# Kernel optimization log

Measured on AMD Instinct MI355X. Metric: run time of the kernel, lower is better.

Reference implementation:

```python
import jax, jax.numpy as jnp
import numpy as np

# dims
B, S, T, F = 8, 1024, 32, 64       # batch, stocks(nodes), seq_len, feature
DWV = 64                            # d_word_vec == d_model
RNN = 64                            # GRU hidden (rnn_unit)
NHID = 128                          # n_hid
NH, DK, DV = 4, 16, 16              # heads, d_k, d_v
NC, NE = 2, 128                     # n_class, num hyperedges (H.shape[1])


def setup_inputs() -> dict:
    key = jax.random.key(0)
    ks = jax.random.split(key, 24)
    def p(i, shape):
        return jax.random.normal(ks[i], shape, jnp.float32) / np.float32(np.sqrt(shape[-1]))
    return {
        'src_seq': jax.random.normal(ks[0], (B, S, T, F), jnp.float32),
        'H': jax.random.normal(ks[1], (S, NE), jnp.float32) * 0.1,
        'adj': jax.random.normal(ks[2], (S, S), jnp.float32) * 0.02,
        'n_hid': NHID,
        # GCN (feature -> n_hid -> feature), shared across both adj and H_new branches
        'gcn_W1': p(3, (F, NHID)), 'gcn_b1': jnp.zeros((NHID,), jnp.float32),
        'gcn_W2': p(4, (NHID, F)), 'gcn_b2': jnp.zeros((F,), jnp.float32),
        # Linear(H.shape[1] -> H.shape[0]) created inside forward
        'Wm': p(5, (S, NE)) * 0.1, 'bm': jnp.zeros((S,), jnp.float32),
        # Linear(feature -> d_word_vec)
        'Wl': p(6, (DWV, F)), 'bl': jnp.zeros((DWV,), jnp.float32),
        # 2-layer GRU (batch_first), torch layout W_{ir|iz|in} stacked
        'Wx0': p(7, (3 * RNN, DWV)), 'Wh0': p(8, (3 * RNN, RNN)),
        'bx0': jnp.zeros((3 * RNN,), jnp.float32), 'bh0': jnp.zeros((3 * RNN,), jnp.float32),
        'Wx1': p(9, (3 * RNN, RNN)), 'Wh1': p(10, (3 * RNN, RNN)),
        'bx1': jnp.zeros((3 * RNN,), jnp.float32), 'bh1': jnp.zeros((3 * RNN,), jnp.float32),
        # temporal multi-head attention
        'Wq': p(11, (NH * DK, RNN)), 'Wk': p(12, (NH * DK, RNN)), 'Wv': p(13, (NH * DV, RNN)),
        'Wo': p(14, (RNN, NH * DV)),
        'ln_g': jnp.ones((RNN,), jnp.float32), 'ln_b': jnp.zeros((RNN,), jnp.float32),
        # HGN: two graph-conv layers over stocks, (T*RNN -> n_hid -> n_hid)
        'Wg1': p(15, (T * RNN, NHID)), 'Wg2': p(16, (NHID, NHID)),
        # tgt_word_prj: n_hid -> n_class (no bias)
        'Wp': p(17, (NC, NHID)),
    }


def reference(src_seq, H, adj, n_hid, gcn_W1, gcn_b1, gcn_W2, gcn_b2, Wm, bm,
              Wl, bl, Wx0, Wh0, bx0, bh0, Wx1, Wh1, bx1, bh1,
              Wq, Wk, Wv, Wo, ln_g, ln_b, Wg1, Wg2, Wp):
    b, s, t, f = src_seq.shape

    # per-timestep GCN over the stock (node) axis, fully batched (replaces the
    # double Python loop of mm+spmm in the original)
    def gcn(x, A):  # x: (b,s,t,f), A: (s,s)
        h = jax.nn.relu(jnp.einsum('nm,bmth->bnth', A, x @ gcn_W1) + gcn_b1)
        return jnp.einsum('nm,bmtf->bntf', A, h @ gcn_W2) + gcn_b2

    H_new = H @ Wm.T + bm                       # (s,s) learned hypergraph adjacency
    z = gcn(src_seq, adj) + gcn(src_seq, H_new)  # y_i + y_f for all timesteps

    x = (z @ Wl.T + bl).reshape(b * s, t, -1)    # (N, T, DWV)
    n = b * s

    def gru_layer(xin, Wx, Wh, bx, bh):
        hdim = Wh.shape[1]
        xp = xin @ Wx.T + bx                      # precompute input projections (N,T,3H)
        def step(h, xt):
            gh = h @ Wh.T + bh
            xr, xz, xn = jnp.split(xt, 3, -1)
            hr, hz, hn = jnp.split(gh, 3, -1)
            r = jax.nn.sigmoid(xr + hr)
            zg = jax.nn.sigmoid(xz + hz)
            cand = jnp.tanh(xn + r * hn)
            hnew = (1.0 - zg) * cand + zg * h
            return hnew, hnew
        h0 = jnp.zeros((xin.shape[0], hdim), xin.dtype)
        _, ys = jax.lax.scan(step, h0, jnp.swapaxes(xp, 0, 1))
        return jnp.swapaxes(ys, 0, 1)

    r = gru_layer(gru_layer(x, Wx0, Wh0, bx0, bh0), Wx1, Wh1, bx1, bh1)  # (N,T,RNN)

    # temporal multi-head self-attention with causal (subsequent) mask
    q = (r @ Wq.T).reshape(n, t, NH, DK)
    k = (r @ Wk.T).reshape(n, t, NH, DK)
    v = (r @ Wv.T).reshape(n, t, NH, DV)
    scores = jnp.einsum('nqhd,nkhd->nhqk', q, k) / np.float32(np.sqrt(DK))
    causal = jnp.triu(jnp.ones((t, t), bool), 1)
    attn = jax.nn.softmax(jnp.where(causal, jnp.float32(-1e9), scores), -1)
    o = jnp.einsum('nhqk,nkhd->nqhd', attn, v).reshape(n, t, NH * DV) @ Wo.T + r
    mu = o.mean(-1, keepdims=True)
    o = (o - mu) / jnp.sqrt(o.var(-1, keepdims=True) + 1e-6) * ln_g + ln_b

    enc = o.reshape(b, s, t * o.shape[-1])        # (b, s, T*RNN)

    # HGN: two graph convolutions over the stock axis -> (b, s, n_hid)
    hg = jax.nn.relu(jnp.einsum('nm,bmd->bnd', adj, enc @ Wg1))
    hg = jnp.einsum('nm,bmd->bnd', adj, hg @ Wg2)

    return hg.reshape(b * s, -1) @ Wp.T           # x_logit_scale = 1.0 (no weight sharing)
```

## Files before the change

kernel.cpp:

```cpp
#include <hip/hip_runtime.h>

typedef __attribute__((ext_vector_type(8))) short bf8;
typedef __attribute__((ext_vector_type(4))) float f4;

__device__ __forceinline__ ushort f2b(float f) {
  union { float f; unsigned u; } v; v.f = f;
  unsigned u = v.u + 0x7FFFu + ((v.u >> 16) & 1u);
  return (ushort)(u >> 16);
}
__device__ __forceinline__ float b2f(ushort h) {
  union { unsigned u; float f; } v; v.u = ((unsigned)h) << 16; return v.f;
}
__device__ __forceinline__ bf8 pack8(const float* p) {
  f4 a = *(const f4*)p; f4 b = *(const f4*)(p + 4);
  bf8 t;
  t[0] = (short)f2b(a[0]); t[1] = (short)f2b(a[1]);
  t[2] = (short)f2b(a[2]); t[3] = (short)f2b(a[3]);
  t[4] = (short)f2b(b[0]); t[5] = (short)f2b(b[1]);
  t[6] = (short)f2b(b[2]); t[7] = (short)f2b(b[3]);
  return t;
}
__device__ __forceinline__ float sigm(float x) { return 1.f / (1.f + __expf(-x)); }
__device__ __forceinline__ float tanh_f(float x) {
  float a = fabsf(x), e = __expf(-2.f * a);
  return copysignf((1.f - e) / (1.f + e), x);
}

__device__ __forceinline__ void gl16(const void* g, void* l) {
  __builtin_amdgcn_global_load_lds(
      (const __attribute__((address_space(1))) unsigned int*)(uintptr_t)g,
      (__attribute__((address_space(3))) unsigned int*)(uintptr_t)l, 16, 0, 0);
}

#define SFENCE __builtin_amdgcn_sched_barrier(0)
#define RAWBAR { __builtin_amdgcn_s_barrier(); SFENCE; }
#define WAIT_LGKM0 { asm volatile("s_waitcnt lgkmcnt(0)" ::: "memory"); SFENCE; }
#define WAIT_VM(n) { asm volatile("s_waitcnt vmcnt(" #n ")" ::: "memory"); SFENCE; }

__global__ __launch_bounds__(256) void cvt_k(const float* __restrict__ in,
                                             ushort* __restrict__ out, int n4) {
  int i = blockIdx.x * 256 + threadIdx.x;
  if (i < n4) {
    f4 v = ((const f4*)in)[i];
    ushort4 o;
    o.x = f2b(v[0]); o.y = f2b(v[1]); o.z = f2b(v[2]); o.w = f2b(v[3]);
    ((ushort4*)out)[i] = o;
  }
}

__global__ __launch_bounds__(256) void cvtT_k(const float* __restrict__ in,
                                              ushort* __restrict__ out, int R, int C) {
  __shared__ ushort t[64][68];
  const int tid = threadIdx.x;
  const int r0 = blockIdx.x * 64, c0 = blockIdx.y * 64;
  #pragma unroll
  for (int it = 0; it < 4; ++it) {
    int r = (tid >> 4) + 16 * it, c = (tid & 15) * 4;
    f4 v = *(const f4*)(in + (long)(r0 + r) * C + c0 + c);
    #pragma unroll
    for (int j = 0; j < 4; ++j) t[c + j][r] = f2b(v[j]);
  }
  __syncthreads();
  #pragma unroll
  for (int it = 0; it < 4; ++it) {
    int cc = (tid >> 4) + 16 * it, rr = (tid & 15) * 4;
    ushort4 o = { t[cc][rr], t[cc][rr + 1], t[cc][rr + 2], t[cc][rr + 3] };
    *(ushort4*)(out + (long)(c0 + cc) * R + r0 + rr) = o;
  }
}

__global__ __launch_bounds__(256) void cat_k(const ushort* __restrict__ a,
                                             const ushort* __restrict__ h,
                                             ushort* __restrict__ o) {
  int i = blockIdx.x * 256 + threadIdx.x;
  int s = i >> 7, c8 = (i & 127) << 3;
  *(int4*)(o + (long)s * 2048 + c8) = *(const int4*)(a + (long)s * 1024 + c8);
  *(int4*)(o + (long)s * 2048 + 1024 + c8) = *(const int4*)(h + (long)s * 1024 + c8);
}

__global__ void wcombT_k(const float* __restrict__ Wl, const float* __restrict__ W2,
                         ushort* __restrict__ out) {
  int idx = blockIdx.x * 256 + threadIdx.x;
  int d = idx >> 7, h = idx & 127;
  float s = 0.f;
  #pragma unroll
  for (int f = 0; f < 64; ++f) s += Wl[d * 64 + f] * W2[h * 64 + f];
  out[d * 128 + h] = f2b(s);
}
__global__ void biasc_k(const float* __restrict__ gb2, const float* __restrict__ Wl,
                        const float* __restrict__ bl, float* __restrict__ bc) {
  int d = threadIdx.x;
  float s = 0.f;
  #pragma unroll
  for (int f = 0; f < 64; ++f) s += gb2[f] * Wl[d * 64 + f];
  bc[d] = 2.f * s + bl[d];
}
__global__ void wfin_k(const float* __restrict__ Wg2, const float* __restrict__ Wp,
                       float* __restrict__ wf) {
  int idx = threadIdx.x;
  int d = idx >> 1, c = idx & 1;
  float s = 0.f;
  #pragma unroll
  for (int e = 0; e < 128; ++e) s += Wg2[d * 128 + e] * Wp[c * 128 + e];
  wf[idx] = s;
}

template<int BIASMODE, int RELU, int OUTMODE>
__global__ __launch_bounds__(512, 2) void gemm3_k(
    const ushort* __restrict__ A, const ushort* __restrict__ B,
    ushort* __restrict__ C, const float* __restrict__ bias, int biasMask,
    int N, int K, int lda, int ldb, int ldc,
    long sAq, long sBq, long sCq)
{
  __shared__ __align__(16) ushort As[2 * 256 * 64];
  __shared__ __align__(16) ushort Bs[2 * 256 * 64];
  const int tid = threadIdx.x, lane = tid & 63, wv = tid >> 6;
  const int wm = wv >> 2, wn = wv & 3;
  const long bm = (long)blockIdx.x * 256, bn = (long)blockIdx.y * 256;
  const int z = blockIdx.z;
  const ushort* Ap = A + (long)z * sAq + bm * lda;
  const ushort* Bp = B + (long)z * sBq + bn * ldb;
  ushort* Cp = C + (long)z * sCq;
  const int nt = K >> 6;

  const int srow = wv * 32 + (lane >> 3);
  const int scol = ((lane & 7) ^ (srow & 7)) << 3;
  const ushort* apb = Ap + (long)srow * lda + scol;
  const ushort* bpb = Bp + (long)srow * ldb + scol;

  #define STAGE3(T, D) { \
    const ushort* ap_ = apb + (T) * 64; \
    const ushort* bp_ = bpb + (T) * 64; \
    ushort* la_ = &As[(D) * 16384 + (wv * 32) * 64]; \
    ushort* lb_ = &Bs[(D) * 16384 + (wv * 32) * 64]; \
    _Pragma("unroll") \
    for (int i_ = 0; i_ < 4; ++i_) gl16(ap_ + (long)(i_ * 8) * lda, la_ + i_ * 512); \
    _Pragma("unroll") \
    for (int i_ = 0; i_ < 4; ++i_) gl16(bp_ + (long)(i_ * 8) * ldb, lb_ + i_ * 512); \
  }

  STAGE3(0, 0);
  if (nt > 1) { STAGE3(1, 1); WAIT_VM(8); }
  else        { WAIT_VM(0); }
  RAWBAR;

  f4 acc[8][4] = {};
  for (int t = 0; t < nt; ++t) {
    const int d = t & 1;
    const ushort* as = As + d * 16384;
    const ushort* bs = Bs + d * 16384;
    bf8 b0[4], a0[8];
    #pragma unroll
    for (int n = 0; n < 4; ++n) {
      int r = wn * 64 + n * 16 + (lane & 15);
      b0[n] = *(const bf8*)(bs + r * 64 + (((lane >> 4) ^ (r & 7)) << 3));
    }
    #pragma unroll
    for (int m = 0; m < 8; ++m) {
      int r = wm * 128 + m * 16 + (lane & 15);
      a0[m] = *(const bf8*)(as + r * 64 + (((lane >> 4) ^ (r & 7)) << 3));
    }
    __builtin_amdgcn_s_setprio(1);
    #pragma unroll
    for (int m = 0; m < 8; ++m)
      #pragma unroll
      for (int n = 0; n < 4; ++n)
        acc[m][n] = __builtin_amdgcn_mfma_f32_16x16x32_bf16(a0[m], b0[n], acc[m][n], 0, 0, 0);
    __builtin_amdgcn_s_setprio(0);
    bf8 b1[4], a1[8];
    #pragma unroll
    for (int n = 0; n < 4; ++n) {
      int r = wn * 64 + n * 16 + (lane & 15);
      b1[n] = *(const bf8*)(bs + r * 64 + (((4 + (lane >> 4)) ^ (r & 7)) << 3));
    }
    #pragma unroll
    for (int m = 0; m < 8; ++m) {
      int r = wm * 128 + m * 16 + (lane & 15);
      a1[m] = *(const bf8*)(as + r * 64 + (((4 + (lane >> 4)) ^ (r & 7)) << 3));
    }
    WAIT_LGKM0;
    RAWBAR;
    if (t + 2 < nt) STAGE3(t + 2, d);
    __builtin_amdgcn_s_setprio(1);
    #pragma unroll
    for (int m = 0; m < 8; ++m)
      #pragma unroll
      for (int n = 0; n < 4; ++n)
        acc[m][n] = __builtin_amdgcn_mfma_f32_16x16x32_bf16(a1[m], b1[n], acc[m][n], 0, 0, 0);
    __builtin_amdgcn_s_setprio(0);
    if (t + 1 < nt) {
      if (t + 2 < nt) { WAIT_VM(8); }
      else            { WAIT_VM(0); }
      RAWBAR;
    }
  }
  #undef STAGE3

  #pragma unroll
  for (int m = 0; m < 8; ++m) {
    int grow = (int)bm + wm * 128 + m * 16 + ((lane >> 4) << 2);
    #pragma unroll
    for (int n = 0; n < 4; ++n) {
      int col = (int)bn + wn * 64 + n * 16 + (lane & 15);
      if (OUTMODE == 2) {
        int hh = grow & 127, tt = grow >> 7;
        ushort4 o;
        o.x = f2b(acc[m][n][0]); o.y = f2b(acc[m][n][1]);
        o.z = f2b(acc[m][n][2]); o.w = f2b(acc[m][n][3]);
        *(ushort4*)(Cp + ((long)col * 32 + tt) * 128 + hh) = o;
      } else {
        #pragma unroll
        for (int rr = 0; rr < 4; ++rr) {
          float v = acc[m][n][rr];
          if (BIASMODE == 1) v += bias[col & biasMask];
          if (BIASMODE == 2) v += bias[(grow + rr) & biasMask];
          if (RELU) v = fmaxf(v, 0.f);
          Cp[(long)(grow + rr) * ldc + col] = f2b(v);
        }
      }
    }
  }
}

template<int BIASMODE, int RELU, int OUTMODE, int SWZ>
__global__ __launch_bounds__(256) void gemm2_k(
    const ushort* __restrict__ A, const ushort* __restrict__ B,
    ushort* __restrict__ C, const float* __restrict__ bias, int biasMask,
    int N, int K, int lda, int ldb, int ldc, int ZD,
    long sAq, long sAr, long sBq, long sBr, long sCq, long sCr)
{
  __shared__ __align__(16) ushort As[2 * 128 * 64];
  __shared__ __align__(16) ushort Bs[2 * 128 * 64];
  const int tid = threadIdx.x, lane = tid & 63, wv = tid >> 6;
  const int wm = wv >> 1, wn = wv & 1;
  int bx = blockIdx.x, by = blockIdx.y;
  const long bm = (long)bx * 128, bn = (long)by * 128;
  int z = blockIdx.z, zq = z, zr = 0;
  if (ZD > 1) { zq = z / ZD; zr = z - zq * ZD; }
  const ushort* Ap = A + (long)zq * sAq + (long)zr * sAr + bm * lda;
  const ushort* Bp = B + (long)zq * sBq + (long)zr * sBr + bn * ldb;
  ushort* Cp = C + (long)zq * sCq + (long)zr * sCr;
  const int nt = K >> 6;

  const int srow = wv * 32 + (lane >> 3);
  const int scol = ((lane & 7) ^ (srow & 7)) << 3;
  const ushort* apb = Ap + (long)srow * lda + scol;
  const ushort* bpb = Bp + (long)srow * ldb + scol;

  #define STAGE(T, D) { \
    const ushort* ap_ = apb + (T) * 64; \
    const ushort* bp_ = bpb + (T) * 64; \
    ushort* la_ = &As[((D) * 128 + wv * 32) * 64]; \
    ushort* lb_ = &Bs[((D) * 128 + wv * 32) * 64]; \
    _Pragma("unroll") \
    for (int i_ = 0; i_ < 4; ++i_) gl16(ap_ + (long)(i_ * 8) * lda, la_ + i_ * 512); \
    _Pragma("unroll") \
    for (int i_ = 0; i_ < 4; ++i_) gl16(bp_ + (long)(i_ * 8) * ldb, lb_ + i_ * 512); \
  }

  STAGE(0, 0);
  if (nt > 1) { STAGE(1, 1); WAIT_VM(8); }
  else        { WAIT_VM(0); }
  RAWBAR;

  f4 acc[4][4] = {};
  for (int t = 0; t < nt; ++t) {
    const int d = t & 1;
    const ushort* as = As + d * 8192;
    const ushort* bs = Bs + d * 8192;
    bf8 af[4][2], bfv[4][2];
    #pragma unroll
    for (int mi = 0; mi < 4; ++mi) {
      int r = wm * 64 + mi * 16 + (lane & 15);
      #pragma unroll
      for (int kk = 0; kk < 2; ++kk) {
        int blk = kk * 4 + (lane >> 4);
        af[mi][kk] = *(const bf8*)(as + r * 64 + ((blk ^ (r & 7)) << 3));
      }
    }
    #pragma unroll
    for (int ni = 0; ni < 4; ++ni) {
      int r = wn * 64 + ni * 16 + (lane & 15);
      #pragma unroll
      for (int kk = 0; kk < 2; ++kk) {
        int blk = kk * 4 + (lane >> 4);
        bfv[ni][kk] = *(const bf8*)(bs + r * 64 + ((blk ^ (r & 7)) << 3));
      }
    }
    WAIT_LGKM0;
    RAWBAR;
    if (t + 2 < nt) STAGE(t + 2, d);
    #pragma unroll
    for (int kk = 0; kk < 2; ++kk)
      #pragma unroll
      for (int mi = 0; mi < 4; ++mi)
        #pragma unroll
        for (int ni = 0; ni < 4; ++ni)
          acc[mi][ni] = __builtin_amdgcn_mfma_f32_16x16x32_bf16(af[mi][kk], bfv[ni][kk], acc[mi][ni], 0, 0, 0);
    if (t + 1 < nt) {
      if (t + 2 < nt) { WAIT_VM(8); }
      else            { WAIT_VM(0); }
      RAWBAR;
    }
  }
  #undef STAGE

  #pragma unroll
  for (int mi = 0; mi < 4; ++mi)
    #pragma unroll
    for (int ni = 0; ni < 4; ++ni) {
      int col = (int)bn + wn * 64 + ni * 16 + (lane & 15);
      if (col < N) {
        if (OUTMODE == 2) {
          int hh = wm * 64 + mi * 16 + (lane >> 4) * 4;
          int tt = (int)(bm >> 7);
          ushort4 o;
          o.x = f2b(acc[mi][ni][0]); o.y = f2b(acc[mi][ni][1]);
          o.z = f2b(acc[mi][ni][2]); o.w = f2b(acc[mi][ni][3]);
          *(ushort4*)(Cp + ((long)col * 32 + tt) * 128 + hh) = o;
        } else {
          #pragma unroll
          for (int rr = 0; rr < 4; ++rr) {
            int row = (int)bm + wm * 64 + mi * 16 + (lane >> 4) * 4 + rr;
            float v = acc[mi][ni][rr];
            if (BIASMODE == 1) v += bias[col & biasMask];
            if (BIASMODE == 2) v += bias[row & biasMask];
            if (RELU) v = fmaxf(v, 0.f);
            Cp[(long)row * ldc + col] = f2b(v);
          }
        }
      }
    }
}

__global__ __launch_bounds__(256) void gemmsk_k(
    const ushort* __restrict__ A, const ushort* __restrict__ B,
    float* __restrict__ P, int Kc, int lda, int ldb,
    long sAq, long sBq)
{
  __shared__ __align__(16) ushort As[2 * 128 * 64];
  __shared__ __align__(16) ushort Bs[2 * 128 * 64];
  const int tid = threadIdx.x, lane = tid & 63, wv = tid >> 6;
  const int wm = wv >> 1, wn = wv & 1;
  const long bm = (long)blockIdx.x * 128, bn = (long)blockIdx.y * 128;
  const int kc = blockIdx.z & 3, zq = blockIdx.z >> 2;
  const ushort* Ap = A + (long)zq * sAq + kc * Kc + bm * lda;
  const ushort* Bp = B + (long)zq * sBq + kc * Kc + bn * ldb;
  const int nt = Kc >> 6;

  const int srow = wv * 32 + (lane >> 3);
  const int scol = ((lane & 7) ^ (srow & 7)) << 3;
  const ushort* apb = Ap + (long)srow * lda + scol;
  const ushort* bpb = Bp + (long)srow * ldb + scol;

  #define STAGEK(T, D) { \
    const ushort* ap_ = apb + (T) * 64; \
    const ushort* bp_ = bpb + (T) * 64; \
    ushort* la_ = &As[((D) * 128 + wv * 32) * 64]; \
    ushort* lb_ = &Bs[((D) * 128 + wv * 32) * 64]; \
    _Pragma("unroll") \
    for (int i_ = 0; i_ < 4; ++i_) gl16(ap_ + (long)(i_ * 8) * lda, la_ + i_ * 512); \
    _Pragma("unroll") \
    for (int i_ = 0; i_ < 4; ++i_) gl16(bp_ + (long)(i_ * 8) * ldb, lb_ + i_ * 512); \
  }

  STAGEK(0, 0);
  if (nt > 1) { STAGEK(1, 1); WAIT_VM(8); }
  else        { WAIT_VM(0); }
  RAWBAR;

  f4 acc[4][4] = {};
  for (int t = 0; t < nt; ++t) {
    const int d = t & 1;
    const ushort* as = As + d * 8192;
    const ushort* bs = Bs + d * 8192;
    bf8 af[4][2], bfv[4][2];
    #pragma unroll
    for (int mi = 0; mi < 4; ++mi) {
      int r = wm * 64 + mi * 16 + (lane & 15);
      #pragma unroll
      for (int kk = 0; kk < 2; ++kk) {
        int blk = kk * 4 + (lane >> 4);
        af[mi][kk] = *(const bf8*)(as + r * 64 + ((blk ^ (r & 7)) << 3));
      }
    }
    #pragma unroll
    for (int ni = 0; ni < 4; ++ni) {
      int r = wn * 64 + ni * 16 + (lane & 15);
      #pragma unroll
      for (int kk = 0; kk < 2; ++kk) {
        int blk = kk * 4 + (lane >> 4);
        bfv[ni][kk] = *(const bf8*)(bs + r * 64 + ((blk ^ (r & 7)) << 3));
      }
    }
    WAIT_LGKM0;
    RAWBAR;
    if (t + 2 < nt) STAGEK(t + 2, d);
    #pragma unroll
    for (int kk = 0; kk < 2; ++kk)
      #pragma unroll
      for (int mi = 0; mi < 4; ++mi)
        #pragma unroll
        for (int ni = 0; ni < 4; ++ni)
          acc[mi][ni] = __builtin_amdgcn_mfma_f32_16x16x32_bf16(af[mi][kk], bfv[ni][kk], acc[mi][ni], 0, 0, 0);
    if (t + 1 < nt) {
      if (t + 2 < nt) { WAIT_VM(8); }
      else            { WAIT_VM(0); }
      RAWBAR;
    }
  }
  #undef STAGEK

  float* Pp = P + (long)blockIdx.z * 131072;
  #pragma unroll
  for (int mi = 0; mi < 4; ++mi)
    #pragma unroll
    for (int ni = 0; ni < 4; ++ni) {
      int col = (int)bn + wn * 64 + ni * 16 + (lane & 15);
      #pragma unroll
      for (int rr = 0; rr < 4; ++rr) {
        int row = (int)bm + wm * 64 + mi * 16 + (lane >> 4) * 4 + rr;
        Pp[(long)row * 1024 + col] = acc[mi][ni][rr];
      }
    }
}

template<int RELU>
__global__ __launch_bounds__(256) void redk_k(const float* __restrict__ P,
                                              ushort* __restrict__ C) {
  int idx = blockIdx.x * 256 + threadIdx.x;
  long z = idx >> 15;
  long rem = (long)(idx & 32767) * 4;
  const float* base = P + z * 4 * 131072 + rem;
  f4 s = *(const f4*)base;
  #pragma unroll
  for (int kc = 1; kc < 4; ++kc) s += *(const f4*)(base + kc * 131072);
  ushort4 o;
  #pragma unroll
  for (int j = 0; j < 4; ++j) {
    float v = s[j];
    if (RELU) v = fmaxf(v, 0.f);
    ((ushort*)&o)[j] = f2b(v);
  }
  *(ushort4*)(C + z * 131072 + rem) = o;
}

template<int BIASMODE, int RELU, int FULLB, int OUTMODE, int SWZ>
__global__ __launch_bounds__(256) void gemm_k(
    const ushort* __restrict__ A, const ushort* __restrict__ B,
    ushort* __restrict__ C, const float* __restrict__ bias, int biasMask,
    int N, int K, int lda, int ldb, int ldc, int ZD,
    long sAq, long sAr, long sBq, long sBr, long sCq, long sCr)
{
  __shared__ __align__(16) ushort As[128 * 64];
  __shared__ __align__(16) ushort Bs[128 * 64];
  const int tid = threadIdx.x, lane = tid & 63, wv = tid >> 6;
  const int wm = wv >> 1, wn = wv & 1;
  int bx = blockIdx.x, by = blockIdx.y;
  const long bm = (long)bx * 128, bn = (long)by * 128;
  int z = blockIdx.z, zq = z, zr = 0;
  if (ZD > 1) { zq = z / ZD; zr = z - zq * ZD; }
  const ushort* Ap = A + (long)zq * sAq + (long)zr * sAr + bm * lda;
  const ushort* Bp = B + (long)zq * sBq + (long)zr * sBr + bn * ldb;
  ushort* Cp = C + (long)zq * sCq + (long)zr * sCr;
  f4 acc[4][4] = {};
  for (int k0 = 0; k0 < K; k0 += 64) {
    #pragma unroll
    for (int i = 0; i < 4; ++i) {
      int row = wv * 32 + i * 8 + (lane >> 3);
      int gc = k0 + (((lane & 7) ^ (row & 7)) << 3);
      gl16(Ap + (long)row * lda + gc, &As[(wv * 32 + i * 8) * 64]);
    }
    if (FULLB) {
      #pragma unroll
      for (int i = 0; i < 4; ++i) {
        int row = wv * 32 + i * 8 + (lane >> 3);
        int gc = k0 + (((lane & 7) ^ (row & 7)) << 3);
        gl16(Bp + (long)row * ldb + gc, &Bs[(wv * 32 + i * 8) * 64]);
      }
    } else {
      #pragma unroll
      for (int i = 0; i < 4; ++i) {
        int row = (tid >> 3) + 32 * i;
        int b8 = tid & 7;
        int4 v = {0, 0, 0, 0};
        if (bn + row < N) v = *(const int4*)(Bp + (long)row * ldb + k0 + ((b8 ^ (row & 7)) << 3));
        *(int4*)(&Bs[row * 64 + b8 * 8]) = v;
      }
    }
    __syncthreads();
    bf8 af[4][2], bfv[4][2];
    #pragma unroll
    for (int mi = 0; mi < 4; ++mi) {
      int r = wm * 64 + mi * 16 + (lane & 15);
      #pragma unroll
      for (int kk = 0; kk < 2; ++kk) {
        int blk = kk * 4 + (lane >> 4);
        af[mi][kk] = *(const bf8*)(&As[r * 64 + ((blk ^ (r & 7)) << 3)]);
      }
    }
    #pragma unroll
    for (int ni = 0; ni < 4; ++ni) {
      int r = wn * 64 + ni * 16 + (lane & 15);
      #pragma unroll
      for (int kk = 0; kk < 2; ++kk) {
        int blk = kk * 4 + (lane >> 4);
        bfv[ni][kk] = *(const bf8*)(&Bs[r * 64 + ((blk ^ (r & 7)) << 3)]);
      }
    }
    #pragma unroll
    for (int kk = 0; kk < 2; ++kk)
      #pragma unroll
      for (int mi = 0; mi < 4; ++mi)
        #pragma unroll
        for (int ni = 0; ni < 4; ++ni)
          acc[mi][ni] = __builtin_amdgcn_mfma_f32_16x16x32_bf16(af[mi][kk], bfv[ni][kk], acc[mi][ni], 0, 0, 0);
    __syncthreads();
  }
  #pragma unroll
  for (int mi = 0; mi < 4; ++mi)
    #pragma unroll
    for (int ni = 0; ni < 4; ++ni) {
      int col = (int)bn + wn * 64 + ni * 16 + (lane & 15);
      if (col < N) {
        #pragma unroll
        for (int rr = 0; rr < 4; ++rr) {
          int row = (int)bm + wm * 64 + mi * 16 + (lane >> 4) * 4 + rr;
          float v = acc[mi][ni][rr];
          if (BIASMODE == 1) v += bias[col & biasMask];
          if (BIASMODE == 2) v += bias[row & biasMask];
          if (RELU) v = fmaxf(v, 0.f);
          long oidx;
          if (OUTMODE == 1) oidx = ((long)(row & 31) * 8192 + (row >> 5)) * 64 + col;
          else              oidx = (long)row * ldc + col;
          Cp[oidx] = f2b(v);
        }
      }
    }
}

__global__ __launch_bounds__(256, 2) void gru_k(
    const ushort* __restrict__ xT,
    const float* __restrict__ Wx0, const float* __restrict__ Wh0,
    const float* __restrict__ bx0, const float* __restrict__ bh0,
    const float* __restrict__ Wx1, const float* __restrict__ Wh1,
    const float* __restrict__ bx1, const float* __restrict__ bh1,
    ushort* __restrict__ rout)
{
  __shared__ ushort hbf[2][2][1024];
  const int tid = threadIdx.x, lane = tid & 63, w = tid >> 6;
  const int seq0 = blockIdx.x * 16;
  for (int i = tid; i < 4096; i += 256) ((ushort*)hbf)[i] = 0;

  const float* Wxp[2] = {Wx0, Wx1};
  const float* Whp[2] = {Wh0, Wh1};
  const float* bxp[2] = {bx0, bx1};
  const float* bhp[2] = {bh0, bh1};
  bf8 Wxf[2][3][2], Whf[2][3][2];
  float bxv[2][3], bhv[2][3];
  #pragma unroll
  for (int L = 0; L < 2; ++L)
    #pragma unroll
    for (int g = 0; g < 3; ++g) {
      int row = g * 64 + w * 16 + (lane & 15);
      bxv[L][g] = bxp[L][row];
      bhv[L][g] = bhp[L][row];
      #pragma unroll
      for (int kk = 0; kk < 2; ++kk) {
        int kb = kk * 32 + (lane >> 4) * 8;
        Wxf[L][g][kk] = pack8(Wxp[L] + row * 64 + kb);
        Whf[L][g][kk] = pack8(Whp[L] + row * 64 + kb);
      }
    }
  __syncthreads();

  const int arow = lane & 15;
  const int col = w * 16 + (lane & 15);
  f4 hprev[2] = {{0.f,0.f,0.f,0.f},{0.f,0.f,0.f,0.f}};
  int pv = 0;
  for (int t = 0; t < 32; ++t) {
    const int cur = pv ^ 1;
    #pragma unroll
    for (int L = 0; L < 2; ++L) {
      bf8 axf[2], ahf[2];
      if (L == 0) {
        const ushort* xb = xT + ((long)t * 8192 + seq0 + arow) * 64 + (lane >> 4) * 8;
        axf[0] = *(const bf8*)(xb);
        axf[1] = *(const bf8*)(xb + 32);
      } else {
        #pragma unroll
        for (int kk = 0; kk < 2; ++kk) {
          int blk = kk * 4 + (lane >> 4);
          axf[kk] = *(const bf8*)(&hbf[0][cur][arow * 64 + ((blk ^ (arow & 7)) << 3)]);
        }
      }
      #pragma unroll
      for (int kk = 0; kk < 2; ++kk) {
        int blk = kk * 4 + (lane >> 4);
        ahf[kk] = *(const bf8*)(&hbf[L][pv][arow * 64 + ((blk ^ (arow & 7)) << 3)]);
      }
      f4 aX[3] = {}; f4 aH[3] = {};
      #pragma unroll
      for (int kk = 0; kk < 2; ++kk)
        #pragma unroll
        for (int g = 0; g < 3; ++g) {
          aX[g] = __builtin_amdgcn_mfma_f32_16x16x32_bf16(axf[kk], Wxf[L][g][kk], aX[g], 0, 0, 0);
          aH[g] = __builtin_amdgcn_mfma_f32_16x16x32_bf16(ahf[kk], Whf[L][g][kk], aH[g], 0, 0, 0);
        }
      f4 hn;
      #pragma unroll
      for (int r = 0; r < 4; ++r) {
        float rg = sigm(aX[0][r] + bxv[L][0] + aH[0][r] + bhv[L][0]);
        float zg = sigm(aX[1][r] + bxv[L][1] + aH[1][r] + bhv[L][1]);
        float cand = tanh_f(aX[2][r] + bxv[L][2] + rg * (aH[2][r] + bhv[L][2]));
        hn[r] = (1.f - zg) * cand + zg * hprev[L][r];
      }
      hprev[L] = hn;
      #pragma unroll
      for (int r = 0; r < 4; ++r) {
        int row = (lane >> 4) * 4 + r;
        ushort hb = f2b(hn[r]);
        hbf[L][cur][row * 64 + (((col >> 3) ^ (row & 7)) << 3) + (col & 7)] = hb;
        if (L == 1) rout[((long)(seq0 + row) * 32 + t) * 64 + col] = hb;
      }
      __syncthreads();
    }
    pv = cur;
  }
}

__global__ __launch_bounds__(256) void attn_k(
    const ushort* __restrict__ r,
    const float* __restrict__ Wq, const float* __restrict__ Wk,
    const float* __restrict__ Wv, const float* __restrict__ Wo,
    const float* __restrict__ lng, const float* __restrict__ lnb,
    ushort* __restrict__ enc)
{
  __shared__ ushort q_s[4][32][40];
  __shared__ ushort k_s[4][32][40];
  __shared__ ushort v_s[4][16][40];
  __shared__ ushort p_s[4][32][40];
  __shared__ ushort o_s[32][88];
  __shared__ float  ln_s[32][68];
  const int tid = threadIdx.x, lane = tid & 63, w = tid >> 6;
  const long n = blockIdx.x;

  for (int i = tid; i < 4 * 32 * 40; i += 256) { ((ushort*)q_s)[i] = 0; ((ushort*)k_s)[i] = 0; }

  bf8 wqf[2], wkf[2], wvf[2], wof[2];
  #pragma unroll
  for (int kk = 0; kk < 2; ++kk) {
    int row = w * 16 + (lane & 15);
    int kb = kk * 32 + (lane >> 4) * 8;
    wqf[kk] = pack8(Wq + row * 64 + kb);
    wkf[kk] = pack8(Wk + row * 64 + kb);
    wvf[kk] = pack8(Wv + row * 64 + kb);
    wof[kk] = pack8(Wo + row * 64 + kb);
  }
  __syncthreads();

  bf8 ar[2][2];
  #pragma unroll
  for (int mi = 0; mi < 2; ++mi)
    #pragma unroll
    for (int kk = 0; kk < 2; ++kk)
      ar[mi][kk] = *(const bf8*)(r + (n * 32 + mi * 16 + (lane & 15)) * 64 + kk * 32 + (lane >> 4) * 8);
  f4 aq[2] = {}, ak[2] = {}, av[2] = {};
  #pragma unroll
  for (int kk = 0; kk < 2; ++kk)
    #pragma unroll
    for (int mi = 0; mi < 2; ++mi) {
      aq[mi] = __builtin_amdgcn_mfma_f32_16x16x32_bf16(ar[mi][kk], wqf[kk], aq[mi], 0, 0, 0);
      ak[mi] = __builtin_amdgcn_mfma_f32_16x16x32_bf16(ar[mi][kk], wkf[kk], ak[mi], 0, 0, 0);
      av[mi] = __builtin_amdgcn_mfma_f32_16x16x32_bf16(ar[mi][kk], wvf[kk], av[mi], 0, 0, 0);
    }
  #pragma unroll
  for (int mi = 0; mi < 2; ++mi)
    #pragma unroll
    for (int rr = 0; rr < 4; ++rr) {
      int row = mi * 16 + (lane >> 4) * 4 + rr;
      q_s[w][row][lane & 15] = f2b(aq[mi][rr]);
      k_s[w][row][lane & 15] = f2b(ak[mi][rr]);
      v_s[w][lane & 15][row] = f2b(av[mi][rr]);
    }

  bf8 a_q[2], b_k[2];
  #pragma unroll
  for (int mt = 0; mt < 2; ++mt)
    a_q[mt] = *(const bf8*)(&q_s[w][mt * 16 + (lane & 15)][(lane >> 4) * 8]);
  #pragma unroll
  for (int nt = 0; nt < 2; ++nt)
    b_k[nt] = *(const bf8*)(&k_s[w][nt * 16 + (lane & 15)][(lane >> 4) * 8]);
  f4 s_[2][2] = {};
  #pragma unroll
  for (int mt = 0; mt < 2; ++mt)
    #pragma unroll
    for (int nt = 0; nt < 2; ++nt)
      s_[mt][nt] = __builtin_amdgcn_mfma_f32_16x16x32_bf16(a_q[mt], b_k[nt], s_[mt][nt], 0, 0, 0);
  #pragma unroll
  for (int mt = 0; mt < 2; ++mt)
    #pragma unroll
    for (int rr = 0; rr < 4; ++rr) {
      int trow = mt * 16 + (lane >> 4) * 4 + rr;
      float s0 = s_[mt][0][rr] * 0.25f, s1 = s_[mt][1][rr] * 0.25f;
      int c0 = lane & 15, c1 = 16 + (lane & 15);
      if (c0 > trow) s0 = -1e30f;
      if (c1 > trow) s1 = -1e30f;
      float m = fmaxf(s0, s1);
      #pragma unroll
      for (int d = 1; d < 16; d <<= 1) m = fmaxf(m, __shfl_xor(m, d));
      float e0 = __expf(s0 - m), e1 = __expf(s1 - m);
      float sum = e0 + e1;
      #pragma unroll
      for (int d = 1; d < 16; d <<= 1) sum += __shfl_xor(sum, d);
      float inv = 1.f / sum;
      p_s[w][trow][c0] = f2b(e0 * inv);
      p_s[w][trow][c1] = f2b(e1 * inv);
    }

  bf8 b_v = *(const bf8*)(&v_s[w][lane & 15][(lane >> 4) * 8]);
  f4 o_[2] = {};
  #pragma unroll
  for (int mt = 0; mt < 2; ++mt) {
    bf8 a_p = *(const bf8*)(&p_s[w][mt * 16 + (lane & 15)][(lane >> 4) * 8]);
    o_[mt] = __builtin_amdgcn_mfma_f32_16x16x32_bf16(a_p, b_v, o_[mt], 0, 0, 0);
  }
  #pragma unroll
  for (int mt = 0; mt < 2; ++mt)
    #pragma unroll
    for (int rr = 0; rr < 4; ++rr)
      o_s[mt * 16 + (lane >> 4) * 4 + rr][w * 16 + (lane & 15)] = f2b(o_[mt][rr]);
  __syncthreads();

  bf8 a_o[2][2];
  #pragma unroll
  for (int mt = 0; mt < 2; ++mt)
    #pragma unroll
    for (int kk = 0; kk < 2; ++kk)
      a_o[mt][kk] = *(const bf8*)(&o_s[mt * 16 + (lane & 15)][kk * 32 + (lane >> 4) * 8]);
  f4 oo[2] = {};
  #pragma unroll
  for (int kk = 0; kk < 2; ++kk)
    #pragma unroll
    for (int mt = 0; mt < 2; ++mt)
      oo[mt] = __builtin_amdgcn_mfma_f32_16x16x32_bf16(a_o[mt][kk], wof[kk], oo[mt], 0, 0, 0);
  #pragma unroll
  for (int mt = 0; mt < 2; ++mt)
    #pragma unroll
    for (int rr = 0; rr < 4; ++rr) {
      int row = mt * 16 + (lane >> 4) * 4 + rr;
      int col = w * 16 + (lane & 15);
      float resid = b2f(r[(n * 32 + row) * 64 + col]);
      ln_s[row][col] = oo[mt][rr] + resid;
    }
  __syncthreads();

  {
    int row = tid >> 3, seg = tid & 7;
    float vals[8], sm = 0.f, sq = 0.f;
    #pragma unroll
    for (int j = 0; j < 8; ++j) {
      float v = ln_s[row][seg * 8 + j];
      vals[j] = v; sm += v; sq += v * v;
    }
    #pragma unroll
    for (int d = 1; d < 8; d <<= 1) { sm += __shfl_xor(sm, d); sq += __shfl_xor(sq, d); }
    float mu = sm * (1.f / 64.f);
    float var = sq * (1.f / 64.f) - mu * mu;
    float rs = rsqrtf(var + 1e-6f);
    union { ushort u[8]; int4 v; } ou;
    #pragma unroll
    for (int j = 0; j < 8; ++j) {
      int c = seg * 8 + j;
      ou.u[j] = f2b((vals[j] - mu) * rs * lng[c] + lnb[c]);
    }
    *(int4*)(enc + (n * 32 + row) * 64 + seg * 8) = ou.v;
  }
}

__global__ __launch_bounds__(256) void final2_k(const ushort* __restrict__ hg3aT,
                                                const float* __restrict__ wf,
                                                float* __restrict__ out) {
  int i = blockIdx.x * 256 + threadIdx.x;
  int b = i >> 10, s = i & 1023;
  const ushort* base = hg3aT + (long)b * 131072 + s;
  float a0 = 0.f, a1 = 0.f;
  #pragma unroll
  for (int d = 0; d < 128; ++d) {
    float v = b2f(base[d * 1024]);
    a0 += v * wf[2 * d];
    a1 += v * wf[2 * d + 1];
  }
  out[2 * i] = a0; out[2 * i + 1] = a1;
}

extern "C" void kernel_launch(void* const* d_in, const int* in_sizes, int n_in,
                              void* d_out, int out_size, void* d_ws, size_t ws_size,
                              hipStream_t stream) {
  const float* src = (const float*)d_in[0];
  const float* H   = (const float*)d_in[1];
  const float* adj = (const float*)d_in[2];
  const float* gW1 = (const float*)d_in[4];
  const float* gb1 = (const float*)d_in[5];
  const float* gW2 = (const float*)d_in[6];
  const float* gb2 = (const float*)d_in[7];
  const float* Wm  = (const float*)d_in[8];
  const float* bm  = (const float*)d_in[9];
  const float* Wl  = (const float*)d_in[10];
  const float* bl  = (const float*)d_in[11];
  const float* Wx0 = (const float*)d_in[12];
  const float* Wh0 = (const float*)d_in[13];
  const float* bx0 = (const float*)d_in[14];
  const float* bh0 = (const float*)d_in[15];
  const float* Wx1 = (const float*)d_in[16];
  const float* Wh1 = (const float*)d_in[17];
  const float* bx1 = (const float*)d_in[18];
  const float* bh1 = (const float*)d_in[19];
  const float* Wq  = (const float*)d_in[20];
  const float* Wk  = (const float*)d_in[21];
  const float* Wv  = (const float*)d_in[22];
  const float* Wo  = (const float*)d_in[23];
  const float* lng = (const float*)d_in[24];
  const float* lnb = (const float*)d_in[25];
  const float* Wg1 = (const float*)d_in[26];
  const float* Wg2 = (const float*)d_in[27];
  const float* Wp  = (const float*)d_in[28];

  char* ws = (char*)d_ws;
  const size_t MB = 1048576ull;
  ushort* adj_bf  = (ushort*)(ws);
  ushort* Hnew_bf = (ushort*)(ws + 2 * MB);
  ushort* H_bf    = (ushort*)(ws + 4 * MB);
  ushort* Wm_bf   = (ushort*)(ws + 4 * MB + 262144);
  ushort* W1T     = (ushort*)(ws + 4 * MB + 524288);
  ushort* WcT     = (ushort*)(ws + 4 * MB + 524288 + 16384);
  float*  bc      = (float*) (ws + 4 * MB + 524288 + 32768);
  float*  wfin    = (float*) (ws + 4 * MB + 524288 + 33792);
  ushort* Wg1T    = (ushort*)(ws + 5 * MB);
  ushort* src_bf  = (ushort*)(ws + 6 * MB);
  ushort* adjcat  = (ushort*)(ws + 6 * MB);
  ushort* XT      = (ushort*)(ws + 38 * MB);
  ushort* Psum    = (ushort*)(ws + 38 * MB);
  float*  Pk      = (float*) (ws + 38 * MB);
  ushort* h1cat   = (ushort*)(ws + 102 * MB);
  ushort* enc     = (ushort*)(ws + 102 * MB);
  ushort* g1T     = (ushort*)(ws + 134 * MB);
  ushort* hgT     = (ushort*)(ws + 136 * MB);
  ushort* hg3aT   = (ushort*)(ws + 138 * MB);
  ushort* xT      = (ushort*)(ws + 166 * MB);
  ushort* r_bf    = (ushort*)(ws + 198 * MB);

  auto CVT = [&](const float* in, ushort* out, int n) {
    int n4 = n >> 2;
    cvt_k<<<dim3((n4 + 255) / 256), dim3(256), 0, stream>>>(in, out, n4);
  };
  CVT(src, src_bf, 16777216);
  CVT(adj, adj_bf, 1048576);
  CVT(H, H_bf, 131072);
  CVT(Wm, Wm_bf, 131072);
  cvtT_k<<<dim3(1, 2), 256, 0, stream>>>(gW1, W1T, 64, 128);
  cvtT_k<<<dim3(32, 2), 256, 0, stream>>>(Wg1, Wg1T, 2048, 128);
  wcombT_k<<<dim3(32), 256, 0, stream>>>(Wl, gW2, WcT);
  biasc_k<<<dim3(1), 64, 0, stream>>>(gb2, Wl, bl, bc);
  wfin_k<<<dim3(1), 256, 0, stream>>>(Wg2, Wp, wfin);

  gemm2_k<1,0,0,0><<<dim3(8,8,1),256,0,stream>>>(H_bf, Wm_bf, Hnew_bf, bm, 1023,
      1024, 128, 128, 128, 1024, 1, 0,0, 0,0, 0,0);
  gemm2_k<0,0,0,0><<<dim3(1,8,256),256,0,stream>>>(W1T, src_bf, XT, nullptr, 0,
      1024, 64, 64, 2048, 1024, 32, 0,0, 2097152,64, 4194304,131072);
  cat_k<<<dim3(512),256,0,stream>>>(adj_bf, Hnew_bf, adjcat);
  gemm3_k<2,1,0><<<dim3(16,8,8),512,0,stream>>>(XT, adj_bf, h1cat, gb1, 127,
      2048, 1024, 1024, 1024, 2048, 4194304, 0, 8388608);
  gemm3_k<0,0,2><<<dim3(16,4,8),512,0,stream>>>(h1cat, adjcat, Psum, nullptr, 0,
      1024, 2048, 2048, 2048, 0, 8388608, 0, 4194304);
  gemm_k<1,0,0,1,0><<<dim3(2048,1,1),256,0,stream>>>(Psum, WcT, xT, bc, 63,
      64, 128, 128, 128, 64, 1, 0,0, 0,0, 0,0);
  gru_k<<<dim3(512),dim3(256),0,stream>>>(xT, Wx0,Wh0,bx0,bh0, Wx1,Wh1,bx1,bh1, r_bf);
  attn_k<<<dim3(8192),dim3(256),0,stream>>>(r_bf, Wq,Wk,Wv,Wo, lng,lnb, enc);
  gemmsk_k<<<dim3(1,8,32),256,0,stream>>>(Wg1T, enc, Pk, 512, 2048, 2048, 0, 2097152);
  redk_k<0><<<dim3(1024),256,0,stream>>>(Pk, g1T);
  gemmsk_k<<<dim3(1,8,32),256,0,stream>>>(g1T, adj_bf, Pk, 256, 1024, 1024, 131072, 0);
  redk_k<1><<<dim3(1024),256,0,stream>>>(Pk, hgT);
  gemmsk_k<<<dim3(1,8,32),256,0,stream>>>(hgT, adj_bf, Pk, 256, 1024, 1024, 131072, 0);
  redk_k<0><<<dim3(1024),256,0,stream>>>(Pk, hg3aT);
  final2_k<<<dim3(32),256,0,stream>>>(hg3aT, wfin, (float*)d_out);
}
```

Measured before the change: 610.8 us.

## Fuse Wc projection into gemm3 epilogue, dropping Psum intermediate and gemm_k

The second gemm3 launch now has an OUTMODE 3 epilogue. It writes its accumulator tile to LDS, multiplies it by the combined WcT weights with MFMA, adds the bias and stores straight into the GRU input layout xT. This removes the bf16 Psum round trip through global memory and one kernel launch. The cost is extra LDS traffic, a barrier and more register pressure in the big GEMM's epilogue. The workspace buffers are also reshuffled.

```diff
diff --git a/kernel.cpp b/kernel.cpp
--- a/kernel.cpp
+++ b/kernel.cpp
@@ -110,7 +110,8 @@
     const ushort* __restrict__ A, const ushort* __restrict__ B,
     ushort* __restrict__ C, const float* __restrict__ bias, int biasMask,
     int N, int K, int lda, int ldb, int ldc,
-    long sAq, long sBq, long sCq)
+    long sAq, long sBq, long sCq,
+    const ushort* __restrict__ Wc, const float* __restrict__ bcp)
 {
   __shared__ __align__(16) ushort As[2 * 256 * 64];
   __shared__ __align__(16) ushort Bs[2 * 256 * 64];
@@ -196,19 +197,67 @@
   }
   #undef STAGE3
 
-  #pragma unroll
-  for (int m = 0; m < 8; ++m) {
-    int grow = (int)bm + wm * 128 + m * 16 + ((lane >> 4) << 2);
-    #pragma unroll
-    for (int n = 0; n < 4; ++n) {
-      int col = (int)bn + wn * 64 + n * 16 + (lane & 15);
-      if (OUTMODE == 2) {
-        int hh = grow & 127, tt = grow >> 7;
-        ushort4 o;
-        o.x = f2b(acc[m][n][0]); o.y = f2b(acc[m][n][1]);
-        o.z = f2b(acc[m][n][2]); o.w = f2b(acc[m][n][3]);
-        *(ushort4*)(Cp + ((long)col * 32 + tt) * 128 + hh) = o;
-      } else {
+  if (OUTMODE == 3) {
+    ushort* Ps = (wm == 0) ? (ushort*)As : (ushort*)Bs;
+    #pragma unroll
+    for (int m = 0; m < 8; ++m) {
+      int hq = m * 16 + ((lane >> 4) << 2);
+      #pragma unroll
+      for (int n = 0; n < 4; ++n) {
+        int s = wn * 64 + n * 16 + (lane & 15);
+        int key = (s & 7) << 4;
+        #pragma unroll
+        for (int rr = 0; rr < 4; ++rr)
+          Ps[s * 128 + ((hq + rr) ^ key)] = f2b(acc[m][n][rr]);
+      }
+    }
+    WAIT_LGKM0;
+    RAWBAR;
+    const int tl = wm, sq = wn;
+    const ushort* Pw = (tl == 0) ? (const ushort*)As : (const ushort*)Bs;
+    const int sbase = sq * 64;
+    f4 xacc[4][4] = {};
+    #pragma unroll
+    for (int kk = 0; kk < 4; ++kk) {
+      bf8 pa[4], wb[4];
+      int hq = kk * 32 + ((lane >> 4) << 3);
+      #pragma unroll
+      for (int mt = 0; mt < 4; ++mt) {
+        int s = sbase + mt * 16 + (lane & 15);
+        pa[mt] = *(const bf8*)(Pw + s * 128 + (hq ^ ((s & 7) << 4)));
+      }
+      #pragma unroll
+      for (int ntt = 0; ntt < 4; ++ntt) {
+        int dd = ntt * 16 + (lane & 15);
+        wb[ntt] = *(const bf8*)(Wc + dd * 128 + hq);
+      }
+      #pragma unroll
+      for (int mt = 0; mt < 4; ++mt)
+        #pragma unroll
+        for (int ntt = 0; ntt < 4; ++ntt)
+          xacc[mt][ntt] = __builtin_amdgcn_mfma_f32_16x16x32_bf16(pa[mt], wb[ntt], xacc[mt][ntt], 0, 0, 0);
+    }
+    const int tg = (int)(bm >> 7) + tl;
+    #pragma unroll
+    for (int mt = 0; mt < 4; ++mt)
+      #pragma unroll
+      for (int ntt = 0; ntt < 4; ++ntt) {
+        int dd = ntt * 16 + (lane & 15);
+        float bb = bcp[dd];
+        #pragma unroll
+        for (int rr = 0; rr < 4; ++rr) {
+          int s = sbase + mt * 16 + ((lane >> 4) << 2) + rr;
+          long seq = (long)z * 1024 + bn + s;
+          C[((long)tg * 8192 + seq) * 64 + dd] = f2b(xacc[mt][ntt][rr] + bb);
+        }
+      }
+  } else {
+    #pragma unroll
+    for (int m = 0; m < 8; ++m) {
+      int grow = (int)bm + wm * 128 + m * 16 + ((lane >> 4) << 2);
+      #pragma unroll
+      for (int n = 0; n < 4; ++n) {
+        int col = (int)bn + wn * 64 + n * 16 + (lane & 15);
         #pragma unroll
         for (int rr = 0; rr < 4; ++rr) {
           float v = acc[m][n][rr];
@@ -443,100 +492,6 @@
     ((ushort*)&o)[j] = f2b(v);
   }
   *(ushort4*)(C + z * 131072 + rem) = o;
-}
-
-template<int BIASMODE, int RELU, int FULLB, int OUTMODE, int SWZ>
-__global__ __launch_bounds__(256) void gemm_k(
-    const ushort* __restrict__ A, const ushort* __restrict__ B,
-    ushort* __restrict__ C, const float* __restrict__ bias, int biasMask,
-    int N, int K, int lda, int ldb, int ldc, int ZD,
-    long sAq, long sAr, long sBq, long sBr, long sCq, long sCr)
-{
-  __shared__ __align__(16) ushort As[128 * 64];
-  __shared__ __align__(16) ushort Bs[128 * 64];
-  const int tid = threadIdx.x, lane = tid & 63, wv = tid >> 6;
-  const int wm = wv >> 1, wn = wv & 1;
-  int bx = blockIdx.x, by = blockIdx.y;
-  const long bm = (long)bx * 128, bn = (long)by * 128;
-  int z = blockIdx.z, zq = z, zr = 0;
-  if (ZD > 1) { zq = z / ZD; zr = z - zq * ZD; }
-  const ushort* Ap = A + (long)zq * sAq + (long)zr * sAr + bm * lda;
-  const ushort* Bp = B + (long)zq * sBq + (long)zr * sBr + bn * ldb;
-  ushort* Cp = C + (long)zq * sCq + (long)zr * sCr;
-  f4 acc[4][4] = {};
-  for (int k0 = 0; k0 < K; k0 += 64) {
-    #pragma unroll
-    for (int i = 0; i < 4; ++i) {
-      int row = wv * 32 + i * 8 + (lane >> 3);
-      int gc = k0 + (((lane & 7) ^ (row & 7)) << 3);
-      gl16(Ap + (long)row * lda + gc, &As[(wv * 32 + i * 8) * 64]);
-    }
-    if (FULLB) {
-      #pragma unroll
-      for (int i = 0; i < 4; ++i) {
-        int row = wv * 32 + i * 8 + (lane >> 3);
-        int gc = k0 + (((lane & 7) ^ (row & 7)) << 3);
-        gl16(Bp + (long)row * ldb + gc, &Bs[(wv * 32 + i * 8) * 64]);
-      }
-    } else {
-      #pragma unroll
-      for (int i = 0; i < 4; ++i) {
-        int row = (tid >> 3) + 32 * i;
-        int b8 = tid & 7;
-        int4 v = {0, 0, 0, 0};
-        if (bn + row < N) v = *(const int4*)(Bp + (long)row * ldb + k0 + ((b8 ^ (row & 7)) << 3));
-        *(int4*)(&Bs[row * 64 + b8 * 8]) = v;
-      }
-    }
-    __syncthreads();
-    bf8 af[4][2], bfv[4][2];
-    #pragma unroll
-    for (int mi = 0; mi < 4; ++mi) {
-      int r = wm * 64 + mi * 16 + (lane & 15);
-      #pragma unroll
-      for (int kk = 0; kk < 2; ++kk) {
-        int blk = kk * 4 + (lane >> 4);
-        af[mi][kk] = *(const bf8*)(&As[r * 64 + ((blk ^ (r & 7)) << 3)]);
-      }
-    }
-    #pragma unroll
-    for (int ni = 0; ni < 4; ++ni) {
-      int r = wn * 64 + ni * 16 + (lane & 15);
-      #pragma unroll
-      for (int kk = 0; kk < 2; ++kk) {
-        int blk = kk * 4 + (lane >> 4);
-        bfv[ni][kk] = *(const bf8*)(&Bs[r * 64 + ((blk ^ (r & 7)) << 3)]);
-      }
-    }
-    #pragma unroll
-    for (int kk = 0; kk < 2; ++kk)
-      #pragma unroll
-      for (int mi = 0; mi < 4; ++mi)
-        #pragma unroll
-        for (int ni = 0; ni < 4; ++ni)
-          acc[mi][ni] = __builtin_amdgcn_mfma_f32_16x16x32_bf16(af[mi][kk], bfv[ni][kk], acc[mi][ni], 0, 0, 0);
-    __syncthreads();
-  }
-  #pragma unroll
-  for (int mi = 0; mi < 4; ++mi)
-    #pragma unroll
-    for (int ni = 0; ni < 4; ++ni) {
-      int col = (int)bn + wn * 64 + ni * 16 + (lane & 15);
-      if (col < N) {
-        #pragma unroll
-        for (int rr = 0; rr < 4; ++rr) {
-          int row = (int)bm + wm * 64 + mi * 16 + (lane >> 4) * 4 + rr;
-          float v = acc[mi][ni][rr];
-          if (BIASMODE == 1) v += bias[col & biasMask];
-          if (BIASMODE == 2) v += bias[row & biasMask];
-          if (RELU) v = fmaxf(v, 0.f);
-          long oidx;
-          if (OUTMODE == 1) oidx = ((long)(row & 31) * 8192 + (row >> 5)) * 64 + col;
-          else              oidx = (long)row * ldc + col;
-          Cp[oidx] = f2b(v);
-        }
-      }
-    }
 }
 
 __global__ __launch_bounds__(256, 2) void gru_k(
@@ -840,15 +795,14 @@
   ushort* src_bf  = (ushort*)(ws + 6 * MB);
   ushort* adjcat  = (ushort*)(ws + 6 * MB);
   ushort* XT      = (ushort*)(ws + 38 * MB);
-  ushort* Psum    = (ushort*)(ws + 38 * MB);
-  float*  Pk      = (float*) (ws + 38 * MB);
+  ushort* xT      = (ushort*)(ws + 38 * MB);
+  ushort* r_bf    = (ushort*)(ws + 70 * MB);
   ushort* h1cat   = (ushort*)(ws + 102 * MB);
   ushort* enc     = (ushort*)(ws + 102 * MB);
-  ushort* g1T     = (ushort*)(ws + 134 * MB);
-  ushort* hgT     = (ushort*)(ws + 136 * MB);
-  ushort* hg3aT   = (ushort*)(ws + 138 * MB);
-  ushort* xT      = (ushort*)(ws + 166 * MB);
-  ushort* r_bf    = (ushort*)(ws + 198 * MB);
+  float*  Pk      = (float*) (ws + 134 * MB);
+  ushort* g1T     = (ushort*)(ws + 150 * MB);
+  ushort* hgT     = (ushort*)(ws + 152 * MB);
+  ushort* hg3aT   = (ushort*)(ws + 154 * MB);
 
   auto CVT = [&](const float* in, ushort* out, int n) {
     int n4 = n >> 2;
@@ -870,11 +824,9 @@
       1024, 64, 64, 2048, 1024, 32, 0,0, 2097152,64, 4194304,131072);
   cat_k<<<dim3(512),256,0,stream>>>(adj_bf, Hnew_bf, adjcat);
   gemm3_k<2,1,0><<<dim3(16,8,8),512,0,stream>>>(XT, adj_bf, h1cat, gb1, 127,
-      2048, 1024, 1024, 1024, 2048, 4194304, 0, 8388608);
-  gemm3_k<0,0,2><<<dim3(16,4,8),512,0,stream>>>(h1cat, adjcat, Psum, nullptr, 0,
-      1024, 2048, 2048, 2048, 0, 8388608, 0, 4194304);
-  gemm_k<1,0,0,1,0><<<dim3(2048,1,1),256,0,stream>>>(Psum, WcT, xT, bc, 63,
-      64, 128, 128, 128, 64, 1, 0,0, 0,0, 0,0);
+      2048, 1024, 1024, 1024, 2048, 4194304, 0, 8388608, nullptr, nullptr);
+  gemm3_k<0,0,3><<<dim3(16,4,8),512,0,stream>>>(h1cat, adjcat, xT, nullptr, 0,
+      1024, 2048, 2048, 2048, 0, 8388608, 0, 0, WcT, bc);
   gru_k<<<dim3(512),dim3(256),0,stream>>>(xT, Wx0,Wh0,bx0,bh0, Wx1,Wh1,bx1,bh1, r_bf);
   attn_k<<<dim3(8192),dim3(256),0,stream>>>(r_bf, Wq,Wk,Wv,Wo, lng,lnb, enc);
   gemmsk_k<<<dim3(1,8,32),256,0,stream>>>(Wg1T, enc, Pk, 512, 2048, 2048, 0, 2097152);
```

Measured after the change: 586.0 us. -4.1%, faster.
